# Performance work log

Hardware: AMD Instinct MI355X
Metric: run time of the kernel (lower is better)

The kernel has to match this reference:

```python
import jax, jax.numpy as jnp
import numpy as np

P = 2  # pooling_size

def setup_inputs() -> dict:
    key = jax.random.key(0)
    k1, k2, k3 = jax.random.split(key, 3)
    B, n, D = 16, 4096, 1024
    x = jax.random.normal(k1, (B, n, D), dtype=jnp.float32)
    W1 = jax.random.normal(k2, (D, D), dtype=jnp.float32) * (1.0 / np.sqrt(D))
    b1 = jnp.zeros((D,), dtype=jnp.float32)
    W2 = jax.random.normal(k3, (D, 1), dtype=jnp.float32) * (1.0 / np.sqrt(D))
    b2 = jnp.zeros((1,), dtype=jnp.float32)
    return {"x": x, "W1": W1, "b1": b1, "W2": W2, "b2": b2}

def reference(x, W1, b1, W2, b2):
    # x: [B, n, D] with n a perfect square; pool 2x2 windows via attention.
    B, n, D = x.shape
    s = int(n ** 0.5)
    g = s // P  # grid of regions per side
    # [B, g, P, g, P, D] -> [B, g, g, P, P, D] -> [B, R, P*P, D]
    # region order matches the original double loop (row-major over i, j).
    xg = (x.reshape(B, g, P, g, P, D)
            .transpose(0, 1, 3, 2, 4, 5)
            .reshape(B, g * g, P * P, D))
    # MLP scores (dropout is identity in eval mode)
    h = jax.nn.relu(jnp.einsum('brkd,de->brke', xg, W1) + b1)
    logits = jnp.einsum('brkd,d->brk', h, W2[:, 0]) + b2[0]
    alpha = jax.nn.softmax(logits, axis=-1)  # softmax over the P*P window
    # weighted sum over window -> [B, R, D]
    return jnp.einsum('brk,brkd->brd', alpha, xg)
```

## Files before the change

kernel.cpp:

```cpp
#include <hip/hip_runtime.h>
#include <hip/hip_bf16.h>

typedef float f32x4 __attribute__((ext_vector_type(4)));
typedef __bf16 bf16x8 __attribute__((ext_vector_type(8)));
typedef unsigned short ushort_t;

#define GLDS16(gp, lp)                                                        \
  __builtin_amdgcn_global_load_lds(                                           \
      (__attribute__((address_space(1))) void*)(gp),                          \
      (__attribute__((address_space(3))) void*)(lp), 16, 0, 0)

__device__ __forceinline__ ushort_t f2bf(float f) {
  unsigned u = __float_as_uint(f);
  unsigned r = u + 0x7fffu + ((u >> 16) & 1u);
  return (ushort_t)(r >> 16);
}

__global__ __launch_bounds__(256) void prep_w1(const float* __restrict__ w1,
                                               ushort_t* __restrict__ w1t) {
  __shared__ ushort_t tile[64][80];
  const int k0 = blockIdx.x * 64;
  const int n0 = blockIdx.y * 64;
  const int tid = threadIdx.x;
#pragma unroll
  for (int it = 0; it < 16; ++it) {
    int idx = it * 256 + tid;
    int k = idx >> 6, n = idx & 63;
    tile[n][k] = f2bf(w1[(size_t)(k0 + k) * 1024 + n0 + n]);
  }
  __syncthreads();
#pragma unroll
  for (int it = 0; it < 2; ++it) {
    int idx = it * 256 + tid;
    int n = idx >> 3, kk = (idx & 7) * 8;
    bf16x8 v = *(const bf16x8*)&tile[n][kk];
    *(bf16x8*)&w1t[(size_t)(n0 + n) * 1024 + k0 + kk] = v;
  }
}

#define BM 128
#define BN 128
#define BK 32
#define NKT 32

__global__ __launch_bounds__(256) void gemm_logits(
    const float* __restrict__ x, const ushort_t* __restrict__ w1t,
    const float* __restrict__ b1, const float* __restrict__ w2,
    float* __restrict__ partial) {
  __shared__ ushort_t As[BM][BK];
  __shared__ ushort_t Bs[BN][BK];
  const int tid = threadIdx.x;
  const int wave = tid >> 6, lane = tid & 63;
  const int quad = lane >> 4, lc = lane & 15;
  const int nblk = blockIdx.x;
  const int mblk = blockIdx.y;
  const int m0 = mblk * BM, n0 = nblk * BN;
  const int wm = (wave & 1) * 64, wn = (wave >> 1) * 64;

  f32x4 acc[4][4] = {};

  const int ar = tid >> 3;
  const int ak = (tid & 7) * 4;
  const float* aptr[4];
  ushort_t* adst[4];
#pragma unroll
  for (int it = 0; it < 4; ++it) {
    aptr[it] = x + (size_t)(m0 + it * 32 + ar) * 1024 + ak;
    adst[it] = &As[it * 32 + ar][ak];
  }
  const int g0 = tid, g1 = 256 + tid;
  const ushort_t* bptr0 = w1t + (size_t)(n0 + (g0 >> 2)) * 1024 + (g0 & 3) * 8;
  const ushort_t* bptr1 = w1t + (size_t)(n0 + (g1 >> 2)) * 1024 + (g1 & 3) * 8;
  ushort_t* bdst0 = &Bs[0][0] + (size_t)g0 * 8;
  ushort_t* bdst1 = &Bs[0][0] + (size_t)g1 * 8;

  for (int kt = 0; kt < NKT; ++kt) {
    const int k0 = kt * BK;
    __syncthreads();
    GLDS16(bptr0 + k0, bdst0);
    GLDS16(bptr1 + k0, bdst1);
#pragma unroll
    for (int it = 0; it < 4; ++it) {
      float4 av = *(const float4*)(aptr[it] + k0);
      ushort4 p;
      p.x = f2bf(av.x); p.y = f2bf(av.y); p.z = f2bf(av.z); p.w = f2bf(av.w);
      *(ushort4*)adst[it] = p;
    }
    __syncthreads();

    bf16x8 af[4], bf[4];
#pragma unroll
    for (int mi = 0; mi < 4; ++mi)
      af[mi] = *(const bf16x8*)&As[wm + mi * 16 + lc][quad * 8];
#pragma unroll
    for (int ni = 0; ni < 4; ++ni)
      bf[ni] = *(const bf16x8*)&Bs[wn + ni * 16 + lc][quad * 8];
#pragma unroll
    for (int mi = 0; mi < 4; ++mi)
#pragma unroll
      for (int ni = 0; ni < 4; ++ni)
        acc[mi][ni] = __builtin_amdgcn_mfma_f32_16x16x32_bf16(
            af[mi], bf[ni], acc[mi][ni], 0, 0, 0);
  }

  float bv[4], wv[4];
#pragma unroll
  for (int ni = 0; ni < 4; ++ni) {
    int col = n0 + wn + ni * 16 + lc;
    bv[ni] = b1[col];
    wv[ni] = w2[col];
  }
#pragma unroll
  for (int mi = 0; mi < 4; ++mi) {
    float s0 = 0.f, s1 = 0.f, s2 = 0.f, s3 = 0.f;
#pragma unroll
    for (int ni = 0; ni < 4; ++ni) {
      f32x4 a = acc[mi][ni];
      float h;
      h = a[0] + bv[ni]; h = h > 0.f ? h : 0.f; s0 += h * wv[ni];
      h = a[1] + bv[ni]; h = h > 0.f ? h : 0.f; s1 += h * wv[ni];
      h = a[2] + bv[ni]; h = h > 0.f ? h : 0.f; s2 += h * wv[ni];
      h = a[3] + bv[ni]; h = h > 0.f ? h : 0.f; s3 += h * wv[ni];
    }
#pragma unroll
    for (int off = 1; off < 16; off <<= 1) {
      s0 += __shfl_xor(s0, off, 64);
      s1 += __shfl_xor(s1, off, 64);
      s2 += __shfl_xor(s2, off, 64);
      s3 += __shfl_xor(s3, off, 64);
    }
    if (lc == 0) {
      int rowb = m0 + wm + mi * 16 + quad * 4;
      float* dst =
          partial + (size_t)(nblk * 2 + (wave >> 1)) * 65536 + rowb;
      dst[0] = s0; dst[1] = s1; dst[2] = s2; dst[3] = s3;
    }
  }
}

__global__ __launch_bounds__(256) void pool_out(const float* __restrict__ x,
                                                const float* __restrict__ partial,
                                                const float* __restrict__ b2,
                                                float* __restrict__ out) {
  const int win = blockIdx.x;
  const int b = win >> 10;
  const int r = win & 1023;
  const int i = r >> 5, j = r & 31;
  const int t0 = i * 128 + j * 2;
  const int tid = threadIdx.x;
  __shared__ float sl[4];
  if (tid < 64) {
    const int k = tid >> 4, s = tid & 15;
    const int m = b * 4096 + t0 + (k >> 1) * 64 + (k & 1);
    float v = partial[(size_t)s * 65536 + m];
#pragma unroll
    for (int off = 1; off < 16; off <<= 1) v += __shfl_xor(v, off, 64);
    if (s == 0) sl[k] = v + b2[0];
  }
  __syncthreads();
  float l0 = sl[0], l1 = sl[1], l2 = sl[2], l3 = sl[3];
  float mx = fmaxf(fmaxf(l0, l1), fmaxf(l2, l3));
  float e0 = __expf(l0 - mx), e1 = __expf(l1 - mx);
  float e2 = __expf(l2 - mx), e3 = __expf(l3 - mx);
  float inv = 1.0f / (e0 + e1 + e2 + e3);
  e0 *= inv; e1 *= inv; e2 *= inv; e3 *= inv;

  const size_t base = ((size_t)b * 4096 + t0) * 1024;
  const float4* x0 = (const float4*)(x + base);
  const float4* x1 = (const float4*)(x + base + 1024);
  const float4* x2 = (const float4*)(x + base + 64 * 1024);
  const float4* x3 = (const float4*)(x + base + 65 * 1024);
  float4 v0 = x0[tid], v1 = x1[tid], v2 = x2[tid], v3 = x3[tid];
  float4 o;
  o.x = e0 * v0.x + e1 * v1.x + e2 * v2.x + e3 * v3.x;
  o.y = e0 * v0.y + e1 * v1.y + e2 * v2.y + e3 * v3.y;
  o.z = e0 * v0.z + e1 * v1.z + e2 * v2.z + e3 * v3.z;
  o.w = e0 * v0.w + e1 * v1.w + e2 * v2.w + e3 * v3.w;
  ((float4*)out)[(size_t)win * 256 + tid] = o;
}

extern "C" void kernel_launch(void* const* d_in, const int* in_sizes, int n_in,
                              void* d_out, int out_size, void* d_ws,
                              size_t ws_size, hipStream_t stream) {
  const float* x  = (const float*)d_in[0];
  const float* W1 = (const float*)d_in[1];
  const float* b1 = (const float*)d_in[2];
  const float* W2 = (const float*)d_in[3];
  const float* b2 = (const float*)d_in[4];
  float* out = (float*)d_out;

  ushort_t* w1t = (ushort_t*)d_ws;
  float* partial = (float*)((char*)d_ws + (2u << 20));

  prep_w1<<<dim3(16, 16), 256, 0, stream>>>(W1, w1t);
  gemm_logits<<<dim3(8, 512), 256, 0, stream>>>(x, w1t, b1, W2, partial);
  pool_out<<<dim3(16384), 256, 0, stream>>>(x, partial, b2, out);
}
```

Baseline: 643.1 us.

## Loop all N tiles per block, fuse logit reduction, pre-convert x to bf16

Each GEMM block now owns 128 rows and iterates over all 8 column tiles, accumulating the ReLU·W2 logit in registers and reducing via shared atomics. This removes the 16-way partial buffer and its reduction in the pooling kernel, and avoids re-reading and re-converting fp32 x for every column block. When the workspace is large enough, x is first converted to bf16 in a separate pass so A tiles can be loaded directly into LDS; LDS rows are XOR-swizzled to reduce bank conflicts. The cost is a grid of only 512 blocks with lower parallelism, plus an extra full pass over x for conversion; b2 is dropped since softmax is shift-invariant.

Result: no change. 650.8 us (+1.2%).

```diff
diff --git a/kernel.cpp b/kernel.cpp
--- a/kernel.cpp
+++ b/kernel.cpp
@@ -4,6 +4,7 @@
 typedef float f32x4 __attribute__((ext_vector_type(4)));
 typedef __bf16 bf16x8 __attribute__((ext_vector_type(8)));
 typedef unsigned short ushort_t;
+typedef ushort_t u16x8 __attribute__((ext_vector_type(8)));
 
 #define GLDS16(gp, lp)                                                        \
   __builtin_amdgcn_global_load_lds(                                           \
@@ -14,6 +15,10 @@
   unsigned u = __float_as_uint(f);
   unsigned r = u + 0x7fffu + ((u >> 16) & 1u);
   return (ushort_t)(r >> 16);
+}
+
+__device__ __forceinline__ int swz(int row) {
+  return (row & 3) ^ ((row >> 2) & 3);
 }
 
 __global__ __launch_bounds__(256) void prep_w1(const float* __restrict__ w1,
@@ -38,134 +43,163 @@
   }
 }
 
-#define BM 128
-#define BN 128
-#define BK 32
-#define NKT 32
-
+__global__ __launch_bounds__(256) void prep_x(const float* __restrict__ x,
+                                              ushort_t* __restrict__ xbf) {
+  size_t i = ((size_t)blockIdx.x * 256 + threadIdx.x) * 8;
+  float4 a = *(const float4*)(x + i);
+  float4 b = *(const float4*)(x + i + 4);
+  u16x8 o;
+  o[0] = f2bf(a.x); o[1] = f2bf(a.y); o[2] = f2bf(a.z); o[3] = f2bf(a.w);
+  o[4] = f2bf(b.x); o[5] = f2bf(b.y); o[6] = f2bf(b.z); o[7] = f2bf(b.w);
+  *(u16x8*)(xbf + i) = o;
+}
+
+template <bool A_BF16>
 __global__ __launch_bounds__(256) void gemm_logits(
-    const float* __restrict__ x, const ushort_t* __restrict__ w1t,
+    const void* __restrict__ aglob, const ushort_t* __restrict__ w1t,
     const float* __restrict__ b1, const float* __restrict__ w2,
-    float* __restrict__ partial) {
-  __shared__ ushort_t As[BM][BK];
-  __shared__ ushort_t Bs[BN][BK];
+    float* __restrict__ logits) {
+  __shared__ ushort_t As[128 * 32];
+  __shared__ ushort_t Bs[128 * 32];
   const int tid = threadIdx.x;
   const int wave = tid >> 6, lane = tid & 63;
   const int quad = lane >> 4, lc = lane & 15;
-  const int nblk = blockIdx.x;
-  const int mblk = blockIdx.y;
-  const int m0 = mblk * BM, n0 = nblk * BN;
+  const int m0 = blockIdx.x * 128;
   const int wm = (wave & 1) * 64, wn = (wave >> 1) * 64;
 
-  f32x4 acc[4][4] = {};
-
-  const int ar = tid >> 3;
-  const int ak = (tid & 7) * 4;
-  const float* aptr[4];
-  ushort_t* adst[4];
-#pragma unroll
-  for (int it = 0; it < 4; ++it) {
-    aptr[it] = x + (size_t)(m0 + it * 32 + ar) * 1024 + ak;
-    adst[it] = &As[it * 32 + ar][ak];
-  }
   const int g0 = tid, g1 = 256 + tid;
-  const ushort_t* bptr0 = w1t + (size_t)(n0 + (g0 >> 2)) * 1024 + (g0 & 3) * 8;
-  const ushort_t* bptr1 = w1t + (size_t)(n0 + (g1 >> 2)) * 1024 + (g1 & 3) * 8;
-  ushort_t* bdst0 = &Bs[0][0] + (size_t)g0 * 8;
-  ushort_t* bdst1 = &Bs[0][0] + (size_t)g1 * 8;
-
-  for (int kt = 0; kt < NKT; ++kt) {
-    const int k0 = kt * BK;
-    __syncthreads();
-    GLDS16(bptr0 + k0, bdst0);
-    GLDS16(bptr1 + k0, bdst1);
-#pragma unroll
-    for (int it = 0; it < 4; ++it) {
-      float4 av = *(const float4*)(aptr[it] + k0);
-      ushort4 p;
-      p.x = f2bf(av.x); p.y = f2bf(av.y); p.z = f2bf(av.z); p.w = f2bf(av.w);
-      *(ushort4*)adst[it] = p;
+  const int r0 = g0 >> 2, c0 = (g0 & 3) ^ swz(g0 >> 2);
+  const int r1 = g1 >> 2, c1 = (g1 & 3) ^ swz(g1 >> 2);
+  ushort_t* adst0 = As + g0 * 8;
+  ushort_t* adst1 = As + g1 * 8;
+  ushort_t* bdst0 = Bs + g0 * 8;
+  ushort_t* bdst1 = Bs + g1 * 8;
+  const ushort_t* abf0 = nullptr; const ushort_t* abf1 = nullptr;
+  const float* af32_0 = nullptr; const float* af32_1 = nullptr;
+  if constexpr (A_BF16) {
+    abf0 = (const ushort_t*)aglob + (size_t)(m0 + r0) * 1024 + c0 * 8;
+    abf1 = (const ushort_t*)aglob + (size_t)(m0 + r1) * 1024 + c1 * 8;
+  } else {
+    af32_0 = (const float*)aglob + (size_t)(m0 + r0) * 1024 + c0 * 8;
+    af32_1 = (const float*)aglob + (size_t)(m0 + r1) * 1024 + c1 * 8;
+  }
+  const ushort_t* bbase0 = w1t + (size_t)r0 * 1024 + c0 * 8;
+  const ushort_t* bbase1 = w1t + (size_t)r1 * 1024 + c1 * 8;
+
+  int aoff[4], boff[4];
+#pragma unroll
+  for (int mi = 0; mi < 4; ++mi) {
+    int r = wm + mi * 16 + lc;
+    aoff[mi] = r * 32 + (quad ^ swz(r)) * 8;
+  }
+#pragma unroll
+  for (int ni = 0; ni < 4; ++ni) {
+    int r = wn + ni * 16 + lc;
+    boff[ni] = r * 32 + (quad ^ swz(r)) * 8;
+  }
+
+  float racc[4][4] = {};
+
+  for (int nt = 0; nt < 8; ++nt) {
+    f32x4 acc[4][4] = {};
+    const ushort_t* bp0 = bbase0 + (size_t)nt * 128 * 1024;
+    const ushort_t* bp1 = bbase1 + (size_t)nt * 128 * 1024;
+    for (int kt = 0; kt < 32; ++kt) {
+      const int k0 = kt * 32;
+      __syncthreads();
+      GLDS16(bp0 + k0, bdst0);
+      GLDS16(bp1 + k0, bdst1);
+      if constexpr (A_BF16) {
+        GLDS16(abf0 + k0, adst0);
+        GLDS16(abf1 + k0, adst1);
+      } else {
+        float4 v0 = *(const float4*)(af32_0 + k0);
+        float4 v1 = *(const float4*)(af32_0 + k0 + 4);
+        float4 v2 = *(const float4*)(af32_1 + k0);
+        float4 v3 = *(const float4*)(af32_1 + k0 + 4);
+        u16x8 o0, o1;
+        o0[0] = f2bf(v0.x); o0[1] = f2bf(v0.y); o0[2] = f2bf(v0.z); o0[3] = f2bf(v0.w);
+        o0[4] = f2bf(v1.x); o0[5] = f2bf(v1.y); o0[6] = f2bf(v1.z); o0[7] = f2bf(v1.w);
+        o1[0] = f2bf(v2.x); o1[1] = f2bf(v2.y); o1[2] = f2bf(v2.z); o1[3] = f2bf(v2.w);
+        o1[4] = f2bf(v3.x); o1[5] = f2bf(v3.y); o1[6] = f2bf(v3.z); o1[7] = f2bf(v3.w);
+        *(u16x8*)adst0 = o0;
+        *(u16x8*)adst1 = o1;
+      }
+      __syncthreads();
+
+      bf16x8 afr[4], bfr[4];
+#pragma unroll
+      for (int mi = 0; mi < 4; ++mi) afr[mi] = *(const bf16x8*)&As[aoff[mi]];
+#pragma unroll
+      for (int ni = 0; ni < 4; ++ni) bfr[ni] = *(const bf16x8*)&Bs[boff[ni]];
+#pragma unroll
+      for (int mi = 0; mi < 4; ++mi)
+#pragma unroll
+        for (int ni = 0; ni < 4; ++ni)
+          acc[mi][ni] = __builtin_amdgcn_mfma_f32_16x16x32_bf16(
+              afr[mi], bfr[ni], acc[mi][ni], 0, 0, 0);
     }
-    __syncthreads();
-
-    bf16x8 af[4], bf[4];
+    float bv[4], wv[4];
+#pragma unroll
+    for (int ni = 0; ni < 4; ++ni) {
+      int col = nt * 128 + wn + ni * 16 + lc;
+      bv[ni] = b1[col];
+      wv[ni] = w2[col];
+    }
 #pragma unroll
     for (int mi = 0; mi < 4; ++mi)
-      af[mi] = *(const bf16x8*)&As[wm + mi * 16 + lc][quad * 8];
-#pragma unroll
-    for (int ni = 0; ni < 4; ++ni)
-      bf[ni] = *(const bf16x8*)&Bs[wn + ni * 16 + lc][quad * 8];
+#pragma unroll
+      for (int r = 0; r < 4; ++r) {
+        float s = 0.f;
+#pragma unroll
+        for (int ni = 0; ni < 4; ++ni) {
+          float h = acc[mi][ni][r] + bv[ni];
+          h = h > 0.f ? h : 0.f;
+          s += h * wv[ni];
+        }
+        racc[mi][r] += s;
+      }
+  }
+
+#pragma unroll
+  for (int mi = 0; mi < 4; ++mi)
+#pragma unroll
+    for (int r = 0; r < 4; ++r)
+#pragma unroll
+      for (int off = 1; off < 16; off <<= 1)
+        racc[mi][r] += __shfl_xor(racc[mi][r], off, 64);
+  __syncthreads();
+  float* lbuf = (float*)As;
+  if (tid < 128) lbuf[tid] = 0.f;
+  __syncthreads();
+  if (lc == 0) {
 #pragma unroll
     for (int mi = 0; mi < 4; ++mi)
 #pragma unroll
-      for (int ni = 0; ni < 4; ++ni)
-        acc[mi][ni] = __builtin_amdgcn_mfma_f32_16x16x32_bf16(
-            af[mi], bf[ni], acc[mi][ni], 0, 0, 0);
-  }
-
-  float bv[4], wv[4];
-#pragma unroll
-  for (int ni = 0; ni < 4; ++ni) {
-    int col = n0 + wn + ni * 16 + lc;
-    bv[ni] = b1[col];
-    wv[ni] = w2[col];
-  }
-#pragma unroll
-  for (int mi = 0; mi < 4; ++mi) {
-    float s0 = 0.f, s1 = 0.f, s2 = 0.f, s3 = 0.f;
-#pragma unroll
-    for (int ni = 0; ni < 4; ++ni) {
-      f32x4 a = acc[mi][ni];
-      float h;
-      h = a[0] + bv[ni]; h = h > 0.f ? h : 0.f; s0 += h * wv[ni];
-      h = a[1] + bv[ni]; h = h > 0.f ? h : 0.f; s1 += h * wv[ni];
-      h = a[2] + bv[ni]; h = h > 0.f ? h : 0.f; s2 += h * wv[ni];
-      h = a[3] + bv[ni]; h = h > 0.f ? h : 0.f; s3 += h * wv[ni];
-    }
-#pragma unroll
-    for (int off = 1; off < 16; off <<= 1) {
-      s0 += __shfl_xor(s0, off, 64);
-      s1 += __shfl_xor(s1, off, 64);
-      s2 += __shfl_xor(s2, off, 64);
-      s3 += __shfl_xor(s3, off, 64);
-    }
-    if (lc == 0) {
-      int rowb = m0 + wm + mi * 16 + quad * 4;
-      float* dst =
-          partial + (size_t)(nblk * 2 + (wave >> 1)) * 65536 + rowb;
-      dst[0] = s0; dst[1] = s1; dst[2] = s2; dst[3] = s3;
-    }
-  }
+      for (int r = 0; r < 4; ++r)
+        atomicAdd(&lbuf[wm + mi * 16 + quad * 4 + r], racc[mi][r]);
+  }
+  __syncthreads();
+  if (tid < 128) logits[m0 + tid] = lbuf[tid];
 }
 
 __global__ __launch_bounds__(256) void pool_out(const float* __restrict__ x,
-                                                const float* __restrict__ partial,
-                                                const float* __restrict__ b2,
+                                                const float* __restrict__ logits,
                                                 float* __restrict__ out) {
   const int win = blockIdx.x;
-  const int b = win >> 10;
-  const int r = win & 1023;
+  const int b = win >> 10, r = win & 1023;
   const int i = r >> 5, j = r & 31;
-  const int t0 = i * 128 + j * 2;
+  const int m = b * 4096 + i * 128 + j * 2;
   const int tid = threadIdx.x;
-  __shared__ float sl[4];
-  if (tid < 64) {
-    const int k = tid >> 4, s = tid & 15;
-    const int m = b * 4096 + t0 + (k >> 1) * 64 + (k & 1);
-    float v = partial[(size_t)s * 65536 + m];
-#pragma unroll
-    for (int off = 1; off < 16; off <<= 1) v += __shfl_xor(v, off, 64);
-    if (s == 0) sl[k] = v + b2[0];
-  }
-  __syncthreads();
-  float l0 = sl[0], l1 = sl[1], l2 = sl[2], l3 = sl[3];
+  float l0 = logits[m], l1 = logits[m + 1];
+  float l2 = logits[m + 64], l3 = logits[m + 65];
   float mx = fmaxf(fmaxf(l0, l1), fmaxf(l2, l3));
   float e0 = __expf(l0 - mx), e1 = __expf(l1 - mx);
   float e2 = __expf(l2 - mx), e3 = __expf(l3 - mx);
   float inv = 1.0f / (e0 + e1 + e2 + e3);
   e0 *= inv; e1 *= inv; e2 *= inv; e3 *= inv;
 
-  const size_t base = ((size_t)b * 4096 + t0) * 1024;
+  const size_t base = (size_t)m * 1024;
   const float4* x0 = (const float4*)(x + base);
   const float4* x1 = (const float4*)(x + base + 1024);
   const float4* x2 = (const float4*)(x + base + 64 * 1024);
@@ -186,13 +220,25 @@
   const float* W1 = (const float*)d_in[1];
   const float* b1 = (const float*)d_in[2];
   const float* W2 = (const float*)d_in[3];
-  const float* b2 = (const float*)d_in[4];
   float* out = (float*)d_out;
 
-  ushort_t* w1t = (ushort_t*)d_ws;
-  float* partial = (float*)((char*)d_ws + (2u << 20));
-
-  prep_w1<<<dim3(16, 16), 256, 0, stream>>>(W1, w1t);
-  gemm_logits<<<dim3(8, 512), 256, 0, stream>>>(x, w1t, b1, W2, partial);
-  pool_out<<<dim3(16384), 256, 0, stream>>>(x, partial, b2, out);
-}
+  const size_t XBF_BYTES = 134217728ull;
+  const size_t W1T_BYTES = 2097152ull;
+  const size_t LGT_BYTES = 262144ull;
+
+  if (ws_size >= XBF_BYTES + W1T_BYTES + LGT_BYTES) {
+    ushort_t* xbf = (ushort_t*)d_ws;
+    ushort_t* w1t = (ushort_t*)((char*)d_ws + XBF_BYTES);
+    float* logits = (float*)((char*)d_ws + XBF_BYTES + W1T_BYTES);
+    prep_x<<<32768, 256, 0, stream>>>(x, xbf);
+    prep_w1<<<dim3(16, 16), 256, 0, stream>>>(W1, w1t);
+    gemm_logits<true><<<512, 256, 0, stream>>>(xbf, w1t, b1, W2, logits);
+    pool_out<<<16384, 256, 0, stream>>>(x, logits, out);
+  } else {
+    ushort_t* w1t = (ushort_t*)d_ws;
+    float* logits = (float*)((char*)d_ws + W1T_BYTES);
+    prep_w1<<<dim3(16, 16), 256, 0, stream>>>(W1, w1t);
+    gemm_logits<false><<<512, 256, 0, stream>>>(x, w1t, b1, W2, logits);
+    pool_out<<<16384, 256, 0, stream>>>(x, logits, out);
+  }
+}
```
